# Kernel optimization log

Hardware: AMD Instinct MI355X
Metric: run time of the kernel (lower is better)

Reference implementation:

```python
import jax, jax.numpy as jnp
import numpy as np

N, E, B, DIM = 50000, 800000, 64, 64

def setup_inputs() -> dict:
    key = jax.random.key(0)
    ks = jax.random.split(key, 8)
    x = jax.random.normal(ks[0], (N, DIM), dtype=jnp.float32)
    edge_index = jax.random.randint(ks[1], (2, E), 0, N, dtype=jnp.int64)
    edge_attr = jax.random.normal(ks[2], (E, DIM), dtype=jnp.float32)
    u = jax.random.normal(ks[3], (B, DIM), dtype=jnp.float32)
    batch = jnp.sort(jax.random.randint(ks[4], (N,), 0, B, dtype=jnp.int64))
    # MLP params: Linear(3*dim, dim) -> ReLU -> Linear(dim, dim)
    s1 = 1.0 / np.sqrt(3 * DIM)
    s2 = 1.0 / np.sqrt(DIM)
    W1 = jax.random.uniform(ks[5], (3 * DIM, DIM), minval=-s1, maxval=s1, dtype=jnp.float32)
    b1 = jnp.zeros((DIM,), dtype=jnp.float32)
    W2 = jax.random.uniform(ks[6], (DIM, DIM), minval=-s2, maxval=s2, dtype=jnp.float32)
    b2 = jnp.zeros((DIM,), dtype=jnp.float32)
    return {"x": x, "edge_index": edge_index, "edge_attr": edge_attr, "u": u,
            "batch": batch, "W1": W1, "b1": b1, "W2": W2, "b2": b2}

def reference(x, edge_index, edge_attr, u, batch, W1, b1, W2, b2):
    src = edge_index[0]
    # scatter_mean(edge_attr, src, dim=0) -> [N, DIM]; empty segments give 0
    sums = jax.ops.segment_sum(edge_attr, src, num_segments=N)
    counts = jax.ops.segment_sum(jnp.ones((E,), dtype=edge_attr.dtype), src, num_segments=N)
    v_e = sums / jnp.maximum(counts, 1.0)[:, None]
    comb = jnp.concatenate([x, v_e, u[batch]], axis=1)  # [N, 3*DIM]
    h = jax.nn.relu(comb @ W1 + b1)
    return h @ W2 + b2
```

## Files before the change

### kernel.cpp

```cpp
#include <hip/hip_runtime.h>

#define NN 50000
#define NE 800000
#define NB 64
#define DIM 64
#define TM 128
#define CAP 64
#define EB 4096
#define NBLK_A 196
#define NBKT 196

typedef float vfloat4 __attribute__((ext_vector_type(4)));


__global__ __launch_bounds__(1024) void bucketA_k(const int* __restrict__ src,
                                                  int* __restrict__ bbuf,
                                                  int* __restrict__ blkoff,
                                                  const float* __restrict__ u,
                                                  const float* __restrict__ W1,
                                                  const float* __restrict__ b1,
                                                  float* __restrict__ U1) {
    __shared__ int hist[NBKT];
    __shared__ int cnt2[NBKT];
    __shared__ int off[NBKT + 1];
    __shared__ int sortedE[EB];

    const int tid = threadIdx.x;
    const int blk = blockIdx.x;

    for (int i = tid; i < NBKT; i += 1024) { hist[i] = 0; cnt2[i] = 0; }
    __syncthreads();

    const int e0 = (blk * 1024 + tid) * 4;
    const bool valid = (e0 < NE);
    int4 s4 = make_int4(0, 0, 0, 0);
    if (valid) s4 = ((const int4*)src)[e0 >> 2];
    const int bk0 = s4.x >> 8, bk1 = s4.y >> 8, bk2 = s4.z >> 8, bk3 = s4.w >> 8;

    if (valid) {
        atomicAdd(&hist[bk0], 1);
        atomicAdd(&hist[bk1], 1);
        atomicAdd(&hist[bk2], 1);
        atomicAdd(&hist[bk3], 1);
    }
    __syncthreads();

    if (tid < 64) {
        const int base = tid * 4;
        int a0 = 0, a1 = 0, a2 = 0, a3 = 0;
        if (base < NBKT) {
            a0 = hist[base + 0]; a1 = hist[base + 1];
            a2 = hist[base + 2]; a3 = hist[base + 3];
        }
        const int sum = a0 + a1 + a2 + a3;
        int run = sum;
        #pragma unroll
        for (int m = 1; m < 64; m <<= 1) {
            int v = __shfl_up(run, m, 64);
            if (tid >= m) run += v;
        }
        const int excl = run - sum;
        if (base < NBKT) {
            off[base + 0] = excl;
            off[base + 1] = excl + a0;
            off[base + 2] = excl + a0 + a1;
            off[base + 3] = excl + a0 + a1 + a2;
        }
        if (tid == 63) off[NBKT] = run;
    }
    __syncthreads();

    if (valid) {
        int r0 = off[bk0] + atomicAdd(&cnt2[bk0], 1); sortedE[r0] = e0 + 0;
        int r1 = off[bk1] + atomicAdd(&cnt2[bk1], 1); sortedE[r1] = e0 + 1;
        int r2 = off[bk2] + atomicAdd(&cnt2[bk2], 1); sortedE[r2] = e0 + 2;
        int r3 = off[bk3] + atomicAdd(&cnt2[bk3], 1); sortedE[r3] = e0 + 3;
    }
    __syncthreads();

    const int nE = min(EB, NE - blk * EB);
    for (int i = tid; i < nE; i += 1024)
        bbuf[blk * EB + i] = sortedE[i];
    for (int i = tid; i <= NBKT; i += 1024)
        blkoff[blk * (NBKT + 1) + i] = off[i];

    if (blk < NB && tid < DIM) {
        float a = b1[tid];
        const float* up = u + blk * DIM;
        #pragma unroll 8
        for (int k = 0; k < DIM; ++k)
            a = fmaf(up[k], W1[(2 * DIM + k) * DIM + tid], a);
        U1[blk * DIM + tid] = a;
    }
}

__global__ __launch_bounds__(1024) void placeB_k(const int* __restrict__ src,
                                                 const int* __restrict__ bbuf,
                                                 const int* __restrict__ blkoff,
                                                 int* __restrict__ eids,
                                                 int* __restrict__ deg) {
    __shared__ int cnt[256];
    __shared__ int lo_s[NBLK_A], hi_s[NBLK_A];
    __shared__ int segoff[NBLK_A + 1];

    const int b = blockIdx.x;
    const int tid = threadIdx.x;

    if (tid < 256) cnt[tid] = 0;
    if (tid < NBLK_A) {
        lo_s[tid] = blkoff[tid * (NBKT + 1) + b];
        hi_s[tid] = blkoff[tid * (NBKT + 1) + b + 1];
    }
    __syncthreads();

    if (tid < 64) {
        const int base = tid * 4;
        int a0 = 0, a1 = 0, a2 = 0, a3 = 0;
        if (base < NBLK_A) {
            a0 = hi_s[base + 0] - lo_s[base + 0];
            a1 = hi_s[base + 1] - lo_s[base + 1];
            a2 = hi_s[base + 2] - lo_s[base + 2];
            a3 = hi_s[base + 3] - lo_s[base + 3];
        }
        const int sum = a0 + a1 + a2 + a3;
        int run = sum;
        #pragma unroll
        for (int m = 1; m < 64; m <<= 1) {
            int v = __shfl_up(run, m, 64);
            if (tid >= m) run += v;
        }
        const int excl = run - sum;
        if (base < NBLK_A) {
            segoff[base + 0] = excl;
            segoff[base + 1] = excl + a0;
            segoff[base + 2] = excl + a0 + a1;
            segoff[base + 3] = excl + a0 + a1 + a2;
        }
        if (tid == 63) segoff[NBLK_A] = run;
    }
    __syncthreads();

    const int total = segoff[NBLK_A];
    for (int i = tid; i < total; i += 1024) {
        int lo2 = 0, hi2 = NBLK_A;
        while (lo2 + 1 < hi2) {
            int mid = (lo2 + hi2) >> 1;
            if (segoff[mid] <= i) lo2 = mid; else hi2 = mid;
        }
        const int blk = lo2;
        const int idx = i - segoff[blk] + lo_s[blk];
        const int e = bbuf[blk * EB + idx];
        const int s = src[e];
        const int rank = atomicAdd(&cnt[s & 255], 1);
        eids[s * CAP + rank] = e;
    }
    __syncthreads();

    const int s = b * 256 + tid;
    if (tid < 256 && s < NN) deg[s] = cnt[tid];
}

__global__ __launch_bounds__(256) void reduce_k(const int* __restrict__ deg_arr,
                                                const int* __restrict__ eids,
                                                const vfloat4* __restrict__ ea4,
                                                float4* __restrict__ ve4) {
    int n = (blockIdx.x * 256 + threadIdx.x) >> 6;
    int lane = threadIdx.x & 63;
    int chunk = lane & 15, slot = lane >> 4;
    int deg = deg_arr[n];
    const int* ebase = eids + (size_t)n * CAP;

    vfloat4 acc = {0.f, 0.f, 0.f, 0.f};
    const vfloat4 vzero = {0.f, 0.f, 0.f, 0.f};

    if (deg > 0) {
        int dm1 = deg - 1;
        int e[8];
        #pragma unroll
        for (int r = 0; r < 8; ++r) {
            int j = slot + r * 4;
            e[r] = ebase[j < dm1 ? j : dm1];
        }
        #pragma unroll
        for (int r = 0; r < 8; ++r) {
            vfloat4 v = __builtin_nontemporal_load(&ea4[(size_t)e[r] * 16 + chunk]);
            acc += (slot + r * 4 < deg) ? v : vzero;
        }
        for (int j = 32 + slot; j < deg; j += 4) {
            int ee = ebase[j];
            vfloat4 v = __builtin_nontemporal_load(&ea4[(size_t)ee * 16 + chunk]);
            acc += v;
        }
    }

    #pragma unroll
    for (int m = 16; m <= 32; m <<= 1) {
        acc.x += __shfl_xor(acc.x, m, 64);
        acc.y += __shfl_xor(acc.y, m, 64);
        acc.z += __shfl_xor(acc.z, m, 64);
        acc.w += __shfl_xor(acc.w, m, 64);
    }
    if (slot == 0) {
        float rs = 1.0f / fmaxf((float)deg, 1.0f);
        ve4[(size_t)n * 16 + chunk] = make_float4(acc.x * rs, acc.y * rs, acc.z * rs, acc.w * rs);
    }
}

#define LDA 132

__device__ __forceinline__ void gemm4(float acc[4][4],
                                      const float* __restrict__ A,
                                      const float* __restrict__ Wb,
                                      int NG, int DG) {
    #pragma unroll 4
    for (int k = 0; k < 64; ++k) {
        const float4 w = *(const float4*)&Wb[k * 64 + DG];
        const float4 a = *(const float4*)&A[k * LDA + NG];
        const float av[4] = {a.x, a.y, a.z, a.w};
        const float wv[4] = {w.x, w.y, w.z, w.w};
        #pragma unroll
        for (int i = 0; i < 4; ++i)
            #pragma unroll
            for (int j = 0; j < 4; ++j)
                acc[i][j] = fmaf(av[i], wv[j], acc[i][j]);
    }
}

__global__ __launch_bounds__(512) void mlp_k(const float* __restrict__ x,
                                             const int* __restrict__ batch,
                                             const float* __restrict__ W1,
                                             const float* __restrict__ W2,
                                             const float* __restrict__ b2,
                                             const float* __restrict__ ve,
                                             const float* __restrict__ U1,
                                             float* __restrict__ out) {
    __shared__ float A[64 * LDA];
    __shared__ float Wb[64 * 64];

    const int t = threadIdx.x;
    const int c = t & 15;
    const int rb = t >> 4;
    const int DG = (t & 15) * 4;
    const int NG = (t >> 4) * 4;
    const int n0 = blockIdx.x * TM;

    float acc[4][4];

    #pragma unroll
    for (int i = 0; i < 4; ++i) {
        int n = n0 + NG + i;
        int b = (n < NN) ? batch[n] : 0;
        const float4 uv = *(const float4*)&U1[b * DIM + DG];
        acc[i][0] = uv.x; acc[i][1] = uv.y; acc[i][2] = uv.z; acc[i][3] = uv.w;
    }

    #pragma unroll
    for (int it = 0; it < 4; ++it) {
        int r = rb + it * 32;
        int n = n0 + r;
        float4 v = make_float4(0.f, 0.f, 0.f, 0.f);
        if (n < NN) v = *(const float4*)&x[(size_t)n * DIM + c * 4];
        A[(c * 4 + 0) * LDA + r] = v.x;
        A[(c * 4 + 1) * LDA + r] = v.y;
        A[(c * 4 + 2) * LDA + r] = v.z;
        A[(c * 4 + 3) * LDA + r] = v.w;
    }
    #pragma unroll
    for (int it = 0; it < 2; ++it) {
        int r = rb + it * 32;
        *(float4*)&Wb[r * 64 + c * 4] = *(const float4*)&W1[(size_t)r * DIM + c * 4];
    }
    __syncthreads();
    gemm4(acc, A, Wb, NG, DG);
    __syncthreads();

    #pragma unroll
    for (int it = 0; it < 4; ++it) {
        int r = rb + it * 32;
        int n = n0 + r;
        float4 v = make_float4(0.f, 0.f, 0.f, 0.f);
        if (n < NN) v = *(const float4*)&ve[(size_t)n * DIM + c * 4];
        A[(c * 4 + 0) * LDA + r] = v.x;
        A[(c * 4 + 1) * LDA + r] = v.y;
        A[(c * 4 + 2) * LDA + r] = v.z;
        A[(c * 4 + 3) * LDA + r] = v.w;
    }
    #pragma unroll
    for (int it = 0; it < 2; ++it) {
        int r = rb + it * 32;
        *(float4*)&Wb[r * 64 + c * 4] = *(const float4*)&W1[(size_t)(64 + r) * DIM + c * 4];
    }
    __syncthreads();
    gemm4(acc, A, Wb, NG, DG);

    #pragma unroll
    for (int i = 0; i < 4; ++i)
        #pragma unroll
        for (int j = 0; j < 4; ++j)
            acc[i][j] = fmaxf(acc[i][j], 0.f);

    __syncthreads();

    #pragma unroll
    for (int j = 0; j < 4; ++j) {
        float4 h = make_float4(acc[0][j], acc[1][j], acc[2][j], acc[3][j]);
        *(float4*)&A[(DG + j) * LDA + NG] = h;
    }
    #pragma unroll
    for (int it = 0; it < 2; ++it) {
        int r = rb + it * 32;
        *(float4*)&Wb[r * 64 + c * 4] = *(const float4*)&W2[(size_t)r * DIM + c * 4];
    }
    __syncthreads();

    {
        const float4 bv = *(const float4*)&b2[DG];
        #pragma unroll
        for (int i = 0; i < 4; ++i) {
            acc[i][0] = bv.x; acc[i][1] = bv.y; acc[i][2] = bv.z; acc[i][3] = bv.w;
        }
    }
    gemm4(acc, A, Wb, NG, DG);

    #pragma unroll
    for (int i = 0; i < 4; ++i) {
        int n = n0 + NG + i;
        if (n < NN) {
            float4 o = make_float4(acc[i][0], acc[i][1], acc[i][2], acc[i][3]);
            *(float4*)&out[(size_t)n * DIM + DG] = o;
        }
    }
}

extern "C" void kernel_launch(void* const* d_in, const int* in_sizes, int n_in,
                              void* d_out, int out_size, void* d_ws, size_t ws_size,
                              hipStream_t stream)
{
    const float* x     = (const float*)d_in[0];
    const int*   eidx  = (const int*)d_in[1];
    const float* ea    = (const float*)d_in[2];
    const float* u     = (const float*)d_in[3];
    const int*   batch = (const int*)d_in[4];
    const float* W1    = (const float*)d_in[5];
    const float* b1    = (const float*)d_in[6];
    const float* W2    = (const float*)d_in[7];
    const float* b2    = (const float*)d_in[8];
    float* out = (float*)d_out;

    int*   deg    = (int*)d_ws;
    int*   eids   = deg + NN;
    float* U1     = (float*)(eids + (size_t)NN * CAP);
    float* ve     = U1 + NB * DIM;
    int*   bbuf   = (int*)(ve + (size_t)NN * DIM);
    int*   blkoff = bbuf + (size_t)NBLK_A * EB;

    bucketA_k<<<NBLK_A, 1024, 0, stream>>>(eidx, bbuf, blkoff, u, W1, b1, U1);
    placeB_k<<<NBKT, 1024, 0, stream>>>(eidx, bbuf, blkoff, eids, deg);
    reduce_k<<<(NN * 64) / 256, 256, 0, stream>>>(deg, eids, (const vfloat4*)ea, (float4*)ve);
    mlp_k<<<(NN + TM - 1) / TM, 512, 0, stream>>>(x, batch, W1, W2, b2, ve, U1, out);
}
```

Baseline: 93.64 us.

## Fuse edge-mean gather into MLP kernel, dropping intermediate ve buffer

The separate reduce kernel is removed. Its per-node gather-and-mean of edge attributes now runs inside the MLP kernel, with each wave handling 16 nodes in sequence and writing the means directly into shared memory for the second GEMM. This avoids writing and re-reading the N×64 ve buffer and saves one launch. In exchange, the bandwidth-heavy random gather now runs with far fewer blocks (one per 128 nodes, large LDS footprint), so fewer loads are in flight at once and the gather is less able to hide memory latency.

```diff
diff --git a/kernel.cpp b/kernel.cpp
--- a/kernel.cpp
+++ b/kernel.cpp
@@ -160,52 +160,6 @@
     if (tid < 256 && s < NN) deg[s] = cnt[tid];
 }
 
-__global__ __launch_bounds__(256) void reduce_k(const int* __restrict__ deg_arr,
-                                                const int* __restrict__ eids,
-                                                const vfloat4* __restrict__ ea4,
-                                                float4* __restrict__ ve4) {
-    int n = (blockIdx.x * 256 + threadIdx.x) >> 6;
-    int lane = threadIdx.x & 63;
-    int chunk = lane & 15, slot = lane >> 4;
-    int deg = deg_arr[n];
-    const int* ebase = eids + (size_t)n * CAP;
-
-    vfloat4 acc = {0.f, 0.f, 0.f, 0.f};
-    const vfloat4 vzero = {0.f, 0.f, 0.f, 0.f};
-
-    if (deg > 0) {
-        int dm1 = deg - 1;
-        int e[8];
-        #pragma unroll
-        for (int r = 0; r < 8; ++r) {
-            int j = slot + r * 4;
-            e[r] = ebase[j < dm1 ? j : dm1];
-        }
-        #pragma unroll
-        for (int r = 0; r < 8; ++r) {
-            vfloat4 v = __builtin_nontemporal_load(&ea4[(size_t)e[r] * 16 + chunk]);
-            acc += (slot + r * 4 < deg) ? v : vzero;
-        }
-        for (int j = 32 + slot; j < deg; j += 4) {
-            int ee = ebase[j];
-            vfloat4 v = __builtin_nontemporal_load(&ea4[(size_t)ee * 16 + chunk]);
-            acc += v;
-        }
-    }
-
-    #pragma unroll
-    for (int m = 16; m <= 32; m <<= 1) {
-        acc.x += __shfl_xor(acc.x, m, 64);
-        acc.y += __shfl_xor(acc.y, m, 64);
-        acc.z += __shfl_xor(acc.z, m, 64);
-        acc.w += __shfl_xor(acc.w, m, 64);
-    }
-    if (slot == 0) {
-        float rs = 1.0f / fmaxf((float)deg, 1.0f);
-        ve4[(size_t)n * 16 + chunk] = make_float4(acc.x * rs, acc.y * rs, acc.z * rs, acc.w * rs);
-    }
-}
-
 #define LDA 132
 
 __device__ __forceinline__ void gemm4(float acc[4][4],
@@ -226,26 +180,81 @@
     }
 }
 
-__global__ __launch_bounds__(512) void mlp_k(const float* __restrict__ x,
-                                             const int* __restrict__ batch,
-                                             const float* __restrict__ W1,
-                                             const float* __restrict__ W2,
-                                             const float* __restrict__ b2,
-                                             const float* __restrict__ ve,
-                                             const float* __restrict__ U1,
-                                             float* __restrict__ out) {
+__global__ __launch_bounds__(512) void fused_k(const float* __restrict__ x,
+                                               const int* __restrict__ batch,
+                                               const float* __restrict__ W1,
+                                               const float* __restrict__ W2,
+                                               const float* __restrict__ b2,
+                                               const int* __restrict__ deg,
+                                               const int* __restrict__ eids,
+                                               const vfloat4* __restrict__ ea4,
+                                               const float* __restrict__ U1,
+                                               float* __restrict__ out) {
     __shared__ float A[64 * LDA];
     __shared__ float Wb[64 * 64];
 
     const int t = threadIdx.x;
+    const int wave = t >> 6;
+    const int lane = t & 63;
+    const int chunk = lane & 15, slot = lane >> 4;
     const int c = t & 15;
     const int rb = t >> 4;
     const int DG = (t & 15) * 4;
     const int NG = (t >> 4) * 4;
     const int n0 = blockIdx.x * TM;
 
+    const vfloat4 vzero = {0.f, 0.f, 0.f, 0.f};
+    for (int m = 0; m < 16; ++m) {
+        const int nl = wave * 16 + m;
+        const int n = n0 + nl;
+        vfloat4 acc = vzero;
+        int dg = 0;
+        if (n < NN) {
+            dg = deg[n];
+            const int* ebase = eids + (size_t)n * CAP;
+            if (dg > 0) {
+                const int dm1 = dg - 1;
+                int e[8];
+                #pragma unroll
+                for (int r = 0; r < 8; ++r) {
+                    int j = slot + r * 4;
+                    e[r] = ebase[j < dm1 ? j : dm1];
+                }
+                #pragma unroll
+                for (int r = 0; r < 8; ++r) {
+                    vfloat4 v = __builtin_nontemporal_load(&ea4[(size_t)e[r] * 16 + chunk]);
+                    acc += (slot + r * 4 < dg) ? v : vzero;
+                }
+                for (int j = 32 + slot; j < dg; j += 4) {
+                    int ee = ebase[j];
+                    vfloat4 v = __builtin_nontemporal_load(&ea4[(size_t)ee * 16 + chunk]);
+                    acc += v;
+                }
+            }
+        }
+        #pragma unroll
+        for (int mm = 16; mm <= 32; mm <<= 1) {
+            acc.x += __shfl_xor(acc.x, mm, 64);
+            acc.y += __shfl_xor(acc.y, mm, 64);
+            acc.z += __shfl_xor(acc.z, mm, 64);
+            acc.w += __shfl_xor(acc.w, mm, 64);
+        }
+        if (slot == 0) {
+            const float rs = 1.0f / fmaxf((float)dg, 1.0f);
+            A[(chunk * 4 + 0) * LDA + nl] = acc.x * rs;
+            A[(chunk * 4 + 1) * LDA + nl] = acc.y * rs;
+            A[(chunk * 4 + 2) * LDA + nl] = acc.z * rs;
+            A[(chunk * 4 + 3) * LDA + nl] = acc.w * rs;
+        }
+    }
+
+    #pragma unroll
+    for (int it = 0; it < 2; ++it) {
+        int r = rb + it * 32;
+        *(float4*)&Wb[r * 64 + c * 4] = *(const float4*)&W1[(size_t)(64 + r) * DIM + c * 4];
+    }
+
     float acc[4][4];
-
     #pragma unroll
     for (int i = 0; i < 4; ++i) {
         int n = n0 + NG + i;
@@ -253,6 +262,10 @@
         const float4 uv = *(const float4*)&U1[b * DIM + DG];
         acc[i][0] = uv.x; acc[i][1] = uv.y; acc[i][2] = uv.z; acc[i][3] = uv.w;
     }
+    __syncthreads();
+
+    gemm4(acc, A, Wb, NG, DG);
+    __syncthreads();
 
     #pragma unroll
     for (int it = 0; it < 4; ++it) {
@@ -269,26 +282,6 @@
     for (int it = 0; it < 2; ++it) {
         int r = rb + it * 32;
         *(float4*)&Wb[r * 64 + c * 4] = *(const float4*)&W1[(size_t)r * DIM + c * 4];
-    }
-    __syncthreads();
-    gemm4(acc, A, Wb, NG, DG);
-    __syncthreads();
-
-    #pragma unroll
-    for (int it = 0; it < 4; ++it) {
-        int r = rb + it * 32;
-        int n = n0 + r;
-        float4 v = make_float4(0.f, 0.f, 0.f, 0.f);
-        if (n < NN) v = *(const float4*)&ve[(size_t)n * DIM + c * 4];
-        A[(c * 4 + 0) * LDA + r] = v.x;
-        A[(c * 4 + 1) * LDA + r] = v.y;
-        A[(c * 4 + 2) * LDA + r] = v.z;
-        A[(c * 4 + 3) * LDA + r] = v.w;
-    }
-    #pragma unroll
-    for (int it = 0; it < 2; ++it) {
-        int r = rb + it * 32;
-        *(float4*)&Wb[r * 64 + c * 4] = *(const float4*)&W1[(size_t)(64 + r) * DIM + c * 4];
     }
     __syncthreads();
     gemm4(acc, A, Wb, NG, DG);
@@ -350,12 +343,11 @@
     int*   deg    = (int*)d_ws;
     int*   eids   = deg + NN;
     float* U1     = (float*)(eids + (size_t)NN * CAP);
-    float* ve     = U1 + NB * DIM;
-    int*   bbuf   = (int*)(ve + (size_t)NN * DIM);
+    int*   bbuf   = (int*)(U1 + NB * DIM);
     int*   blkoff = bbuf + (size_t)NBLK_A * EB;
 
     bucketA_k<<<NBLK_A, 1024, 0, stream>>>(eidx, bbuf, blkoff, u, W1, b1, U1);
     placeB_k<<<NBKT, 1024, 0, stream>>>(eidx, bbuf, blkoff, eids, deg);
-    reduce_k<<<(NN * 64) / 256, 256, 0, stream>>>(deg, eids, (const vfloat4*)ea, (float4*)ve);
-    mlp_k<<<(NN + TM - 1) / TM, 512, 0, stream>>>(x, batch, W1, W2, b2, ve, U1, out);
-}
+    fused_k<<<(NN + TM - 1) / TM, 512, 0, stream>>>(x, batch, W1, W2, b2,
+                                                    deg, eids, (const vfloat4*)ea, U1, out);
+}
```

Measured after the change: 96.04 us. 2.6% more time.

## Fuse edge placement and segment reduction into one kernel using shared-memory edge lists

Applied to the files above, without the earlier changes.

Merges the placement kernel and the reduction kernel into one, keeping per-node edge lists and degree counts in shared memory (32 KB) instead of writing the global eids and deg arrays and reading them back. Buckets shrink to 128 nodes (392 buckets) so each block's edge lists fit in LDS, and the scan in bucketA now handles 8 entries per lane. This removes one launch and the global round trip for the edge ids. In exchange each block's gather work grows and LDS use lowers occupancy. Edges past CAP=64 per node are now dropped from the sum while still counted in the mean's divisor.

```diff
diff --git a/kernel.cpp b/kernel.cpp
--- a/kernel.cpp
+++ b/kernel.cpp
@@ -8,7 +8,8 @@
 #define CAP 64
 #define EB 4096
 #define NBLK_A 196
-#define NBKT 196
+#define NBKT 392
+#define BN 128
 
 typedef float vfloat4 __attribute__((ext_vector_type(4)));
 
@@ -35,7 +36,7 @@
     const bool valid = (e0 < NE);
     int4 s4 = make_int4(0, 0, 0, 0);
     if (valid) s4 = ((const int4*)src)[e0 >> 2];
-    const int bk0 = s4.x >> 8, bk1 = s4.y >> 8, bk2 = s4.z >> 8, bk3 = s4.w >> 8;
+    const int bk0 = s4.x >> 7, bk1 = s4.y >> 7, bk2 = s4.z >> 7, bk3 = s4.w >> 7;
 
     if (valid) {
         atomicAdd(&hist[bk0], 1);
@@ -46,25 +47,25 @@
     __syncthreads();
 
     if (tid < 64) {
-        const int base = tid * 4;
-        int a0 = 0, a1 = 0, a2 = 0, a3 = 0;
-        if (base < NBKT) {
-            a0 = hist[base + 0]; a1 = hist[base + 1];
-            a2 = hist[base + 2]; a3 = hist[base + 3];
-        }
-        const int sum = a0 + a1 + a2 + a3;
+        const int base = tid * 8;
+        int a[8];
+        int sum = 0;
+        #pragma unroll
+        for (int i = 0; i < 8; ++i) {
+            a[i] = (base + i < NBKT) ? hist[base + i] : 0;
+            sum += a[i];
+        }
         int run = sum;
         #pragma unroll
         for (int m = 1; m < 64; m <<= 1) {
             int v = __shfl_up(run, m, 64);
             if (tid >= m) run += v;
         }
-        const int excl = run - sum;
-        if (base < NBKT) {
-            off[base + 0] = excl;
-            off[base + 1] = excl + a0;
-            off[base + 2] = excl + a0 + a1;
-            off[base + 3] = excl + a0 + a1 + a2;
+        int acc2 = run - sum;
+        #pragma unroll
+        for (int i = 0; i < 8; ++i) {
+            if (base + i < NBKT) off[base + i] = acc2;
+            acc2 += a[i];
         }
         if (tid == 63) off[NBKT] = run;
     }
@@ -94,19 +95,20 @@
     }
 }
 
-__global__ __launch_bounds__(1024) void placeB_k(const int* __restrict__ src,
-                                                 const int* __restrict__ bbuf,
-                                                 const int* __restrict__ blkoff,
-                                                 int* __restrict__ eids,
-                                                 int* __restrict__ deg) {
-    __shared__ int cnt[256];
+__global__ __launch_bounds__(1024) void placeRed_k(const int* __restrict__ src,
+                                                   const int* __restrict__ bbuf,
+                                                   const int* __restrict__ blkoff,
+                                                   const vfloat4* __restrict__ ea4,
+                                                   float4* __restrict__ ve4) {
+    __shared__ int eids_l[BN * CAP];
+    __shared__ int cnt[BN];
     __shared__ int lo_s[NBLK_A], hi_s[NBLK_A];
     __shared__ int segoff[NBLK_A + 1];
 
     const int b = blockIdx.x;
     const int tid = threadIdx.x;
 
-    if (tid < 256) cnt[tid] = 0;
+    if (tid < BN) cnt[tid] = 0;
     if (tid < NBLK_A) {
         lo_s[tid] = blkoff[tid * (NBKT + 1) + b];
         hi_s[tid] = blkoff[tid * (NBKT + 1) + b + 1];
@@ -151,58 +153,56 @@
         const int idx = i - segoff[blk] + lo_s[blk];
         const int e = bbuf[blk * EB + idx];
         const int s = src[e];
-        const int rank = atomicAdd(&cnt[s & 255], 1);
-        eids[s * CAP + rank] = e;
-    }
-    __syncthreads();
-
-    const int s = b * 256 + tid;
-    if (tid < 256 && s < NN) deg[s] = cnt[tid];
-}
-
-__global__ __launch_bounds__(256) void reduce_k(const int* __restrict__ deg_arr,
-                                                const int* __restrict__ eids,
-                                                const vfloat4* __restrict__ ea4,
-                                                float4* __restrict__ ve4) {
-    int n = (blockIdx.x * 256 + threadIdx.x) >> 6;
-    int lane = threadIdx.x & 63;
-    int chunk = lane & 15, slot = lane >> 4;
-    int deg = deg_arr[n];
-    const int* ebase = eids + (size_t)n * CAP;
-
-    vfloat4 acc = {0.f, 0.f, 0.f, 0.f};
+        const int nl = s & (BN - 1);
+        const int rank = atomicAdd(&cnt[nl], 1);
+        if (rank < CAP) eids_l[nl * CAP + rank] = e;
+    }
+    __syncthreads();
+
+    const int wave = tid >> 6, lane = tid & 63;
+    const int chunk = lane & 15, slot = lane >> 4;
     const vfloat4 vzero = {0.f, 0.f, 0.f, 0.f};
 
-    if (deg > 0) {
-        int dm1 = deg - 1;
-        int e[8];
-        #pragma unroll
-        for (int r = 0; r < 8; ++r) {
-            int j = slot + r * 4;
-            e[r] = ebase[j < dm1 ? j : dm1];
-        }
-        #pragma unroll
-        for (int r = 0; r < 8; ++r) {
-            vfloat4 v = __builtin_nontemporal_load(&ea4[(size_t)e[r] * 16 + chunk]);
-            acc += (slot + r * 4 < deg) ? v : vzero;
-        }
-        for (int j = 32 + slot; j < deg; j += 4) {
-            int ee = ebase[j];
-            vfloat4 v = __builtin_nontemporal_load(&ea4[(size_t)ee * 16 + chunk]);
-            acc += v;
-        }
-    }
-
-    #pragma unroll
-    for (int m = 16; m <= 32; m <<= 1) {
-        acc.x += __shfl_xor(acc.x, m, 64);
-        acc.y += __shfl_xor(acc.y, m, 64);
-        acc.z += __shfl_xor(acc.z, m, 64);
-        acc.w += __shfl_xor(acc.w, m, 64);
-    }
-    if (slot == 0) {
-        float rs = 1.0f / fmaxf((float)deg, 1.0f);
-        ve4[(size_t)n * 16 + chunk] = make_float4(acc.x * rs, acc.y * rs, acc.z * rs, acc.w * rs);
+    #pragma unroll
+    for (int m = 0; m < BN / 16; ++m) {
+        const int nl = wave * (BN / 16) + m;
+        const int n = b * BN + nl;
+        if (n >= NN) break;
+        const int deg = min(cnt[nl], CAP);
+        const int* ebase = eids_l + nl * CAP;
+
+        vfloat4 acc = vzero;
+        if (deg > 0) {
+            const int dm1 = deg - 1;
+            int e[8];
+            #pragma unroll
+            for (int r = 0; r < 8; ++r) {
+                int j = slot + r * 4;
+                e[r] = ebase[j < dm1 ? j : dm1];
+            }
+            #pragma unroll
+            for (int r = 0; r < 8; ++r) {
+                vfloat4 v = __builtin_nontemporal_load(&ea4[(size_t)e[r] * 16 + chunk]);
+                acc += (slot + r * 4 < deg) ? v : vzero;
+            }
+            for (int j = 32 + slot; j < deg; j += 4) {
+                int ee = ebase[j];
+                vfloat4 v = __builtin_nontemporal_load(&ea4[(size_t)ee * 16 + chunk]);
+                acc += v;
+            }
+        }
+        #pragma unroll
+        for (int mm = 16; mm <= 32; mm <<= 1) {
+            acc.x += __shfl_xor(acc.x, mm, 64);
+            acc.y += __shfl_xor(acc.y, mm, 64);
+            acc.z += __shfl_xor(acc.z, mm, 64);
+            acc.w += __shfl_xor(acc.w, mm, 64);
+        }
+        if (slot == 0) {
+            const float rs = 1.0f / fmaxf((float)cnt[nl], 1.0f);
+            ve4[(size_t)n * 16 + chunk] =
+                make_float4(acc.x * rs, acc.y * rs, acc.z * rs, acc.w * rs);
+        }
     }
 }
 
@@ -347,15 +347,12 @@
     const float* b2    = (const float*)d_in[8];
     float* out = (float*)d_out;
 
-    int*   deg    = (int*)d_ws;
-    int*   eids   = deg + NN;
-    float* U1     = (float*)(eids + (size_t)NN * CAP);
-    float* ve     = U1 + NB * DIM;
-    int*   bbuf   = (int*)(ve + (size_t)NN * DIM);
+    float* ve     = (float*)d_ws;
+    float* U1     = ve + (size_t)NN * DIM;
+    int*   bbuf   = (int*)(U1 + NB * DIM);
     int*   blkoff = bbuf + (size_t)NBLK_A * EB;
 
     bucketA_k<<<NBLK_A, 1024, 0, stream>>>(eidx, bbuf, blkoff, u, W1, b1, U1);
-    placeB_k<<<NBKT, 1024, 0, stream>>>(eidx, bbuf, blkoff, eids, deg);
-    reduce_k<<<(NN * 64) / 256, 256, 0, stream>>>(deg, eids, (const vfloat4*)ea, (float4*)ve);
+    placeRed_k<<<NBKT, 1024, 0, stream>>>(eidx, bbuf, blkoff, (const vfloat4*)ea, (float4*)ve);
     mlp_k<<<(NN + TM - 1) / TM, 512, 0, stream>>>(x, batch, W1, W2, b2, ve, U1, out);
 }
```

Result: faster. 89.47 us (-4.4%).
